# Kernel tuning notes

Measured on AMD Instinct MI355X. Metric: run time of the kernel, lower is better.

The kernel has to match this reference:

```python
import jax, jax.numpy as jnp
import numpy as np

D = 28            # matrix_dim = sqrt(word_emb_dim) = sqrt(784)
EMB = D * D       # 784
N_WORDS = 32000


def setup_inputs() -> dict:
    key = jax.random.key(0)
    k1, k2 = jax.random.split(key)
    eye_flat = jnp.eye(D, dtype=jnp.float32).reshape(-1)
    # 'identity' init strategy: N(0, 0.1) + identity on the diagonal
    table = jax.random.normal(k1, (N_WORDS + 1, EMB), dtype=jnp.float32) * 0.1 + eye_flat
    # row 0 is the neutral element (padding) = identity matrix
    table = table.at[0].set(eye_flat)
    sent = jax.random.randint(k2, (2048, 64), 0, N_WORDS + 1, dtype=jnp.int32)
    return {"table": table, "sent": sent}


def reference(table, sent):
    B, S = sent.shape
    # embedding gather -> per-word matrices [B, S, D, D]
    mats = table[sent].reshape(B, S, D, D)
    # continual multiplication: cur = M_0 @ M_1 @ ... @ M_{S-1}
    def step(cur, m):  # cur: [B, D, D], m: [B, D, D]
        return jnp.matmul(cur, m), None
    rest = jnp.moveaxis(mats[:, 1:], 1, 0)  # [S-1, B, D, D]
    out, _ = jax.lax.scan(step, mats[:, 0], rest)
    return out.reshape(B, EMB)
```

## Files before the change

### kernel.cpp

```cpp
#include <hip/hip_runtime.h>
#include <stdint.h>


#define D 28
#define EMB 784
#define SEQ 64
#define NITEMS 2048
#define LPI 7
#define IPW 9
#define RPL 4
#define NCHUNK 28
#define CHUNK_F 256
#define BUF_F (NCHUNK * CHUNK_F)

typedef __attribute__((address_space(3))) uint32_t lds_u32;
typedef const __attribute__((address_space(1))) uint32_t glb_u32;

__device__ __forceinline__ void dma_mat(const float* glane, float* lds0) {
#pragma unroll
  for (int t = 0; t < NCHUNK; ++t)
    __builtin_amdgcn_global_load_lds((glb_u32*)(glane + t * D),
                                     (lds_u32*)(lds0 + t * CHUNK_F), 16, 0, 0);
}

#define MATMUL(Aa, Cc)                                                         \
  do {                                                                         \
    _Pragma("unroll") for (int k = 0; k < D; ++k) {                            \
      _Pragma("unroll") for (int jv = 0; jv < 7; ++jv) {                       \
        float4 m = *(const float4*)(Bs + k * CHUNK_F + 4 * jv);                \
        _Pragma("unroll") for (int r = 0; r < RPL; ++r) {                      \
          float a = Aa[r][k];                                                  \
          if (k == 0) {                                                        \
            Cc[r][4 * jv + 0] = a * m.x;                                       \
            Cc[r][4 * jv + 1] = a * m.y;                                       \
            Cc[r][4 * jv + 2] = a * m.z;                                       \
            Cc[r][4 * jv + 3] = a * m.w;                                       \
          } else {                                                             \
            Cc[r][4 * jv + 0] = fmaf(a, m.x, Cc[r][4 * jv + 0]);               \
            Cc[r][4 * jv + 1] = fmaf(a, m.y, Cc[r][4 * jv + 1]);               \
            Cc[r][4 * jv + 2] = fmaf(a, m.z, Cc[r][4 * jv + 2]);               \
            Cc[r][4 * jv + 3] = fmaf(a, m.w, Cc[r][4 * jv + 3]);               \
          }                                                                    \
        }                                                                      \
      }                                                                        \
    }                                                                          \
  } while (0)

#define STEP(Aa, Cc)                                                           \
  do {                                                                         \
    __builtin_amdgcn_s_waitcnt(0x0f70);           \
    __syncthreads();                                                           \
    MATMUL(Aa, Cc);                                                            \
    __syncthreads();               \
    if (s + 1 < SEG_LEN) {                                                     \
      dma_mat(gn, lds);                                                        \
      int nn = (s + 2 < SEG_LEN) ? s + 2 : SEG_LEN - 1;                        \
      gn = glane(nn);                                                          \
    }                                                                          \
    ++s;                                                                       \
  } while (0)

template <int SEG_LEN, int PSEG, bool GATHER>
__global__ __launch_bounds__(64, 1) void chain_kernel(
    const float* __restrict__ src, const int* __restrict__ sent,
    float* __restrict__ dst, int ntask) {
  __shared__ __align__(16) float lds[BUF_F];

  const int lane = threadIdx.x;
  int slot = lane / LPI;
  int rl = lane - slot * LPI;
  if (slot >= IPW) { slot = IPW - 1; rl = LPI - 1; }
  int task = blockIdx.x * IPW + slot;
  if (task >= ntask) task = ntask - 1;

  const int* sp = nullptr;
  if (GATHER) {
    const int item = task / PSEG;
    const int seg = task - item * PSEG;
    sp = sent + item * SEQ + seg * SEG_LEN;
  }
  auto glane = [&](int s) -> const float* {
    const float* m = GATHER ? src + (size_t)sp[s] * EMB
                            : src + ((size_t)task * SEG_LEN + s) * EMB;
    return m + rl * 4;
  };

  float A0[RPL][D], A1[RPL][D];

  {
    const float* m0 = GATHER ? src + (size_t)sp[0] * EMB
                             : src + (size_t)task * SEG_LEN * EMB;
#pragma unroll
    for (int r = 0; r < RPL; ++r) {
      const float* rp = m0 + (rl * RPL + r) * D;
#pragma unroll
      for (int jv = 0; jv < 7; ++jv) {
        float4 v = *(const float4*)(rp + 4 * jv);
        A0[r][4 * jv + 0] = v.x;
        A0[r][4 * jv + 1] = v.y;
        A0[r][4 * jv + 2] = v.z;
        A0[r][4 * jv + 3] = v.w;
      }
    }
  }

  dma_mat(glane(1), lds);
  const float* gn = glane(SEG_LEN > 2 ? 2 : 1);
  const float* Bs = lds + slot * (LPI * 4);

  int s = 1;
#pragma unroll 1
  for (int p = 0; p < (SEG_LEN - 1) / 2; ++p) {
    STEP(A0, A1);
    STEP(A1, A0);
  }
  STEP(A0, A1);

  {
    float* op = dst + (size_t)task * EMB;
#pragma unroll
    for (int r = 0; r < RPL; ++r) {
      float* rp = op + (rl * RPL + r) * D;
#pragma unroll
      for (int jv = 0; jv < 7; ++jv) {
        *(float4*)(rp + 4 * jv) =
            make_float4(A1[r][4 * jv + 0], A1[r][4 * jv + 1],
                        A1[r][4 * jv + 2], A1[r][4 * jv + 3]);
      }
    }
  }
}

extern "C" void kernel_launch(void* const* d_in, const int* in_sizes, int n_in,
                              void* d_out, int out_size, void* d_ws, size_t ws_size,
                              hipStream_t stream) {
  const float* table = (const float*)d_in[0];
  const int* sent = (const int*)d_in[1];
  float* out = (float*)d_out;

  const size_t need = (size_t)NITEMS * 4 * EMB * sizeof(float);
  if (ws_size >= need) {
    float* p = (float*)d_ws;
    const int ntask1 = NITEMS * 4;
    chain_kernel<16, 4, true><<<(ntask1 + IPW - 1) / IPW, 64, 0, stream>>>(
        table, sent, p, ntask1);
    chain_kernel<4, 1, false><<<(NITEMS + IPW - 1) / IPW, 64, 0, stream>>>(
        p, nullptr, out, NITEMS);
  } else {
    chain_kernel<64, 1, true><<<(NITEMS + IPW - 1) / IPW, 64, 0, stream>>>(
        table, sent, out, NITEMS);
  }
}
```

Before: 262.0 us.

## Split LDS B-matrix into halves to overlap DMA with matmul and drop barriers

The single LDS buffer holding the next matrix is split into two halves. After the first half is consumed, the DMA for the next matrix's first half is issued while the second half is multiplied, and the second half's DMA follows. Fine-grained vmcnt waits replace the two __syncthreads per step, on the basis that the block is a single wavefront. The aim is to hide global-to-LDS latency behind compute and remove barrier stalls. The cost is more intricate waitcnt accounting that depends on the exact order of outstanding loads, and the index prefetch now happens inside the step.

```diff
diff --git a/kernel.cpp b/kernel.cpp
--- a/kernel.cpp
+++ b/kernel.cpp
@@ -9,28 +9,28 @@
 #define LPI 7
 #define IPW 9
 #define RPL 4
-#define NCHUNK 28
+#define HROWS 14
 #define CHUNK_F 256
-#define BUF_F (NCHUNK * CHUNK_F)
+#define HBUF_F (HROWS * CHUNK_F)
 
 typedef __attribute__((address_space(3))) uint32_t lds_u32;
 typedef const __attribute__((address_space(1))) uint32_t glb_u32;
 
-__device__ __forceinline__ void dma_mat(const float* glane, float* lds0) {
+__device__ __forceinline__ void dma_half(const float* gl, float* half) {
 #pragma unroll
-  for (int t = 0; t < NCHUNK; ++t)
-    __builtin_amdgcn_global_load_lds((glb_u32*)(glane + t * D),
-                                     (lds_u32*)(lds0 + t * CHUNK_F), 16, 0, 0);
+  for (int t = 0; t < HROWS; ++t)
+    __builtin_amdgcn_global_load_lds((glb_u32*)(gl + t * D),
+                                     (lds_u32*)(half + t * CHUNK_F), 16, 0, 0);
 }
 
-#define MATMUL(Aa, Cc)                                                         \
+#define MMH(Aa, Cc, Bp, K0)                                                    \
   do {                                                                         \
-    _Pragma("unroll") for (int k = 0; k < D; ++k) {                            \
+    _Pragma("unroll") for (int kk = 0; kk < HROWS; ++kk) {                     \
       _Pragma("unroll") for (int jv = 0; jv < 7; ++jv) {                       \
-        float4 m = *(const float4*)(Bs + k * CHUNK_F + 4 * jv);                \
+        float4 m = *(const float4*)((Bp) + kk * CHUNK_F + 4 * jv);             \
         _Pragma("unroll") for (int r = 0; r < RPL; ++r) {                      \
-          float a = Aa[r][k];                                                  \
-          if (k == 0) {                                                        \
+          float a = Aa[r][(K0) + kk];                                          \
+          if ((K0) + kk == 0) {                                                \
             Cc[r][4 * jv + 0] = a * m.x;                                       \
             Cc[r][4 * jv + 1] = a * m.y;                                       \
             Cc[r][4 * jv + 2] = a * m.z;                                       \
@@ -46,16 +46,26 @@
     }                                                                          \
   } while (0)
 
-#define STEP(Aa, Cc)                                                           \
+#define WAIT_VM0 0x0F70
+#define WAIT_VM14 0x0F7E
+#define WAIT_VM15 0x0F7F
+
+#define STEPX(Aa, Cc, LAST)                                                    \
   do {                                                                         \
-    __builtin_amdgcn_s_waitcnt(0x0f70);           \
-    __syncthreads();                                                           \
-    MATMUL(Aa, Cc);                                                            \
-    __syncthreads();               \
-    if (s + 1 < SEG_LEN) {                                                     \
-      dma_mat(gn, lds);                                                        \
-      int nn = (s + 2 < SEG_LEN) ? s + 2 : SEG_LEN - 1;                        \
-      gn = glane(nn);                                                          \
+    __builtin_amdgcn_s_waitcnt(GATHER ? WAIT_VM15 : WAIT_VM14);   \
+    MMH(Aa, Cc, Blo, 0);                                                       \
+    if (LAST) {                                                                \
+      __builtin_amdgcn_s_waitcnt(WAIT_VM0);           \
+      MMH(Aa, Cc, Bhi, HROWS);                                                 \
+    } else {                                                                   \
+      const float* gnx = GATHER ? src + (size_t)idxn * EMB + rl * 4            \
+                                : src + ((size_t)task * SEG_LEN + s + 1) * EMB \
+                                      + rl * 4;                                \
+      dma_half(gnx, ldsLo);            \
+      __builtin_amdgcn_s_waitcnt(WAIT_VM14);                \
+      MMH(Aa, Cc, Bhi, HROWS);                                                 \
+      dma_half(gnx + HROWS * D, ldsHi);                       \
+      if (GATHER) idxn = spl[(s + 2 < SEG_LEN) ? s + 2 : SEG_LEN - 1];         \
     }                                                                          \
     ++s;                                                                       \
   } while (0)
@@ -64,7 +74,8 @@
 __global__ __launch_bounds__(64, 1) void chain_kernel(
     const float* __restrict__ src, const int* __restrict__ sent,
     float* __restrict__ dst, int ntask) {
-  __shared__ __align__(16) float lds[BUF_F];
+  __shared__ __align__(16) float ldsLo[HBUF_F];
+  __shared__ __align__(16) float ldsHi[HBUF_F];
 
   const int lane = threadIdx.x;
   int slot = lane / LPI;
@@ -73,22 +84,17 @@
   int task = blockIdx.x * IPW + slot;
   if (task >= ntask) task = ntask - 1;
 
-  const int* sp = nullptr;
+  const int* spl = nullptr;
   if (GATHER) {
     const int item = task / PSEG;
     const int seg = task - item * PSEG;
-    sp = sent + item * SEQ + seg * SEG_LEN;
+    spl = sent + item * SEQ + seg * SEG_LEN;
   }
-  auto glane = [&](int s) -> const float* {
-    const float* m = GATHER ? src + (size_t)sp[s] * EMB
-                            : src + ((size_t)task * SEG_LEN + s) * EMB;
-    return m + rl * 4;
-  };
 
   float A0[RPL][D], A1[RPL][D];
 
   {
-    const float* m0 = GATHER ? src + (size_t)sp[0] * EMB
+    const float* m0 = GATHER ? src + (size_t)spl[0] * EMB
                              : src + (size_t)task * SEG_LEN * EMB;
 #pragma unroll
     for (int r = 0; r < RPL; ++r) {
@@ -104,17 +110,25 @@
     }
   }
 
-  dma_mat(glane(1), lds);
-  const float* gn = glane(SEG_LEN > 2 ? 2 : 1);
-  const float* Bs = lds + slot * (LPI * 4);
+  {
+    const float* g1 = GATHER ? src + (size_t)spl[1] * EMB + rl * 4
+                             : src + ((size_t)task * SEG_LEN + 1) * EMB + rl * 4;
+    dma_half(g1, ldsLo);
+    dma_half(g1 + HROWS * D, ldsHi);
+  }
+  int idxn = 0;
+  if (GATHER) idxn = spl[(2 < SEG_LEN) ? 2 : SEG_LEN - 1];
+
+  const float* Blo = ldsLo + slot * (LPI * 4);
+  const float* Bhi = ldsHi + slot * (LPI * 4);
 
   int s = 1;
 #pragma unroll 1
   for (int p = 0; p < (SEG_LEN - 1) / 2; ++p) {
-    STEP(A0, A1);
-    STEP(A1, A0);
+    STEPX(A0, A1, 0);
+    STEPX(A1, A0, 0);
   }
-  STEP(A0, A1);
+  STEPX(A0, A1, 1);
 
   {
     float* op = dst + (size_t)task * EMB;
@@ -138,8 +152,8 @@
   const int* sent = (const int*)d_in[1];
   float* out = (float*)d_out;
 
-  const size_t need = (size_t)NITEMS * 4 * EMB * sizeof(float);
-  if (ws_size >= need) {
+  const size_t need4 = (size_t)NITEMS * 4 * EMB * sizeof(float);
+  if (ws_size >= need4) {
     float* p = (float*)d_ws;
     const int ntask1 = NITEMS * 4;
     chain_kernel<16, 4, true><<<(ntask1 + IPW - 1) / IPW, 64, 0, stream>>>(
```

New measurement: 381.8 us. 1.46x slower.
